# Performance work log

Measured on AMD Instinct MI355X. Metric: run time of the kernel, lower is better.

The kernel has to match this reference:

```python
import jax, jax.numpy as jnp
import numpy as np

N_CLASSES = 91  # classes 0..90; class 0 (background) is excluded from the mean


def setup_inputs() -> dict:
    key = jax.random.key(0)
    k1, k2 = jax.random.split(key)
    B, H, W = 64, 512, 512
    # label maps with integer class ids in [0, 91); `inputs` stored as float32
    # to mirror the original (compared elementwise against integer i)
    inputs = jax.random.randint(k1, (B, H, W), 0, N_CLASSES).astype(jnp.float32)
    targets = jax.random.randint(k2, (B, H, W), 0, N_CLASSES).astype(jnp.int32)
    return {"inputs": inputs, "targets": targets, "smooth": 1}


def reference(inputs, targets, smooth):
    # Single-pass histogram formulation of the original per-class loop:
    #   intersection_i = #{p : inputs[p]==i and targets[p]==i}
    #   total_i        = #{inputs==i} + #{targets==i}
    #   union_i        = total_i - intersection_i
    n = N_CLASSES
    inp = inputs.reshape(-1).astype(jnp.int32)
    tgt = targets.reshape(-1).astype(jnp.int32)
    cnt_in = jnp.bincount(inp, length=n).astype(jnp.float32)
    cnt_tg = jnp.bincount(tgt, length=n).astype(jnp.float32)
    # positions where prediction == target contribute to that class's intersection;
    # mismatches are routed to a dummy bin n and dropped
    inter = jnp.bincount(jnp.where(inp == tgt, inp, n), length=n + 1)[:n].astype(jnp.float32)
    union = cnt_in + cnt_tg - inter
    smooth_f = jnp.float32(smooth)
    iou = (inter[1:] + smooth_f) / (union[1:] + smooth_f)  # classes 1..n-1
    return jnp.sum(iou) / (n - 1)
```

## Files before the change

### kernel.cpp

```cpp
#include <hip/hip_runtime.h>

#define NCLS 91
#define NP (NCLS * NCLS)
#define NHIST (3 * NCLS)
#define NBLK 1024
#define BS 512

__device__ __forceinline__ void proc4(unsigned int* __restrict__ ph, float4 f, int4 t) {
    int a0 = (int)f.x, a1 = (int)f.y, a2 = (int)f.z, a3 = (int)f.w;
    atomicAdd(&ph[a0 * NCLS + t.x], 1u);
    atomicAdd(&ph[a1 * NCLS + t.y], 1u);
    atomicAdd(&ph[a2 * NCLS + t.z], 1u);
    atomicAdd(&ph[a3 * NCLS + t.w], 1u);
}

__global__ __launch_bounds__(BS, 8) void miou_hist(const float* __restrict__ inp,
                                                   const int* __restrict__ tgt,
                                                   unsigned int* __restrict__ ws,
                                                   int n4) {
    __shared__ unsigned int ph[NP];
    for (int i = threadIdx.x; i < NP; i += BS) ph[i] = 0u;
    __syncthreads();

    int tid = blockIdx.x * BS + threadIdx.x;
    int stride = gridDim.x * BS;
    const float4* in4 = (const float4*)inp;
    const int4* tg4 = (const int4*)tgt;

    int i = tid;
    for (; i + stride < n4; i += 2 * stride) {
        float4 f0 = in4[i];
        int4 t0 = tg4[i];
        float4 f1 = in4[i + stride];
        int4 t1 = tg4[i + stride];
        proc4(ph, f0, t0);
        proc4(ph, f1, t1);
    }
    if (i < n4) proc4(ph, in4[i], tg4[i]);
    __syncthreads();

    int t = threadIdx.x;
    if (t < NCLS) {
        unsigned int s = 0;
        const unsigned int* p = ph + t * NCLS;
        for (int k = 0; k < NCLS; ++k) s += p[k];
        if (s) atomicAdd(&ws[t], s);
    } else if (t >= 128 && t < 128 + NCLS) {
        int c = t - 128;
        unsigned int s = 0;
        for (int a = 0; a < NCLS; ++a) s += ph[a * NCLS + c];
        if (s) atomicAdd(&ws[NCLS + c], s);
    } else if (t >= 256 && t < 256 + NCLS) {
        int d = t - 256;
        unsigned int v = ph[d * (NCLS + 1)];
        if (v) atomicAdd(&ws[2 * NCLS + d], v);
    }
}

__global__ void miou_finalize(const unsigned int* __restrict__ ws,
                              const int* __restrict__ smooth_p,
                              float* __restrict__ out) {
    int lane = threadIdx.x;
    float s = (float)(*smooth_p);
    float acc = 0.f;
    for (int c = 1 + lane; c < NCLS; c += 64) {
        float ci = (float)ws[c];
        float ct = (float)ws[NCLS + c];
        float it = (float)ws[2 * NCLS + c];
        float un = ci + ct - it;
        acc += (it + s) / (un + s);
    }
    #pragma unroll
    for (int off = 32; off; off >>= 1) acc += __shfl_down(acc, off);
    if (lane == 0) out[0] = acc / (float)(NCLS - 1);
}

extern "C" void kernel_launch(void* const* d_in, const int* in_sizes, int n_in,
                              void* d_out, int out_size, void* d_ws, size_t ws_size,
                              hipStream_t stream) {
    const float* inp = (const float*)d_in[0];
    const int* tgt = (const int*)d_in[1];
    const int* smooth_p = (const int*)d_in[2];
    float* out = (float*)d_out;
    unsigned int* ws = (unsigned int*)d_ws;

    int n = in_sizes[0];
    int n4 = n >> 2;

    hipMemsetAsync(ws, 0, NHIST * sizeof(unsigned int), stream);
    miou_hist<<<NBLK, BS, 0, stream>>>(inp, tgt, ws, n4);
    miou_finalize<<<1, 64, 0, stream>>>(ws, smooth_p, out);
}
```

Measured before the change: 167.3 us.

## Halve block size, double-buffer batched loads, and restructure histogram reduction

The block size drops to 256 and each thread processes 16 strided float4/int4 pairs, loaded in two register buffers so one batch of global loads is in flight while the previous batch is scattered into the shared 91x91 histogram. Scheduling barriers group the global loads. Zeroing of shared memory is vectorised over a padded array, and the epilogue folds the diagonal extraction into the row-sum threads with 4-way unrolled partial sums. The tradeoff is more register pressure and fewer threads per block contending on the same LDS histogram. The fast path assumes 16*stride covers the data and falls back to a scalar loop otherwise.

```diff
diff --git a/kernel.cpp b/kernel.cpp
--- a/kernel.cpp
+++ b/kernel.cpp
@@ -2,9 +2,10 @@
 
 #define NCLS 91
 #define NP (NCLS * NCLS)
+#define NPPAD 8320
 #define NHIST (3 * NCLS)
 #define NBLK 1024
-#define BS 512
+#define BS 256
 
 __device__ __forceinline__ void proc4(unsigned int* __restrict__ ph, float4 f, int4 t) {
     int a0 = (int)f.x, a1 = (int)f.y, a2 = (int)f.z, a3 = (int)f.w;
@@ -14,46 +15,84 @@
     atomicAdd(&ph[a3 * NCLS + t.w], 1u);
 }
 
-__global__ __launch_bounds__(BS, 8) void miou_hist(const float* __restrict__ inp,
+__global__ __launch_bounds__(BS, 4) void miou_hist(const float* __restrict__ inp,
                                                    const int* __restrict__ tgt,
                                                    unsigned int* __restrict__ ws,
                                                    int n4) {
-    __shared__ unsigned int ph[NP];
-    for (int i = threadIdx.x; i < NP; i += BS) ph[i] = 0u;
+    __shared__ unsigned int ph[NPPAD];
+    uint4* z = (uint4*)ph;
+    #pragma unroll 2
+    for (int i = threadIdx.x; i < NPPAD / 4; i += BS) z[i] = make_uint4(0u, 0u, 0u, 0u);
     __syncthreads();
 
-    int tid = blockIdx.x * BS + threadIdx.x;
-    int stride = gridDim.x * BS;
     const float4* in4 = (const float4*)inp;
     const int4* tg4 = (const int4*)tgt;
+    const int i0 = blockIdx.x * BS + threadIdx.x;
+    const int stride = NBLK * BS;
 
-    int i = tid;
-    for (; i + stride < n4; i += 2 * stride) {
-        float4 f0 = in4[i];
-        int4 t0 = tg4[i];
-        float4 f1 = in4[i + stride];
-        int4 t1 = tg4[i + stride];
-        proc4(ph, f0, t0);
-        proc4(ph, f1, t1);
+    float4 fa0, fa1, fa2, fa3, fb0, fb1, fb2, fb3;
+    int4 ta0, ta1, ta2, ta3, tb0, tb1, tb2, tb3;
+
+#define LOADC(B, C)                                                         \
+    do {                                                                    \
+        int _b = i0 + (C) * 4 * stride;                                     \
+        f##B##0 = in4[_b];              t##B##0 = tg4[_b];                  \
+        f##B##1 = in4[_b + stride];     t##B##1 = tg4[_b + stride];         \
+        f##B##2 = in4[_b + 2 * stride]; t##B##2 = tg4[_b + 2 * stride];     \
+        f##B##3 = in4[_b + 3 * stride]; t##B##3 = tg4[_b + 3 * stride];     \
+        __builtin_amdgcn_sched_group_barrier(0x20, 8, 0);  \
+    } while (0)
+
+#define PROC(B)                                                             \
+    do {                                                                    \
+        proc4(ph, f##B##0, t##B##0);                                        \
+        proc4(ph, f##B##1, t##B##1);                                        \
+        proc4(ph, f##B##2, t##B##2);                                        \
+        proc4(ph, f##B##3, t##B##3);                                        \
+    } while (0)
+
+    int i = i0;
+    if (i0 + 15 * stride < n4) {
+        LOADC(a, 0);
+        LOADC(b, 1);
+        PROC(a);
+        LOADC(a, 2);
+        PROC(b);
+        LOADC(b, 3);
+        PROC(a);
+        PROC(b);
+        i = i0 + 16 * stride;
     }
-    if (i < n4) proc4(ph, in4[i], tg4[i]);
+    for (; i < n4; i += stride) proc4(ph, in4[i], tg4[i]);
+#undef LOADC
+#undef PROC
+
     __syncthreads();
 
     int t = threadIdx.x;
     if (t < NCLS) {
-        unsigned int s = 0;
         const unsigned int* p = ph + t * NCLS;
-        for (int k = 0; k < NCLS; ++k) s += p[k];
+        unsigned int s0 = 0, s1 = 0, s2 = 0, s3 = 0;
+        int k = 0;
+        for (; k + 3 < NCLS; k += 4) { s0 += p[k]; s1 += p[k+1]; s2 += p[k+2]; s3 += p[k+3]; }
+        for (; k < NCLS; ++k) s0 += p[k];
+        unsigned int s = s0 + s1 + s2 + s3;
         if (s) atomicAdd(&ws[t], s);
+        unsigned int d = p[t];
+        if (d) atomicAdd(&ws[2 * NCLS + t], d);
     } else if (t >= 128 && t < 128 + NCLS) {
         int c = t - 128;
-        unsigned int s = 0;
-        for (int a = 0; a < NCLS; ++a) s += ph[a * NCLS + c];
+        unsigned int s0 = 0, s1 = 0, s2 = 0, s3 = 0;
+        int a = 0;
+        for (; a + 3 < NCLS; a += 4) {
+            s0 += ph[a * NCLS + c];
+            s1 += ph[(a + 1) * NCLS + c];
+            s2 += ph[(a + 2) * NCLS + c];
+            s3 += ph[(a + 3) * NCLS + c];
+        }
+        for (; a < NCLS; ++a) s0 += ph[a * NCLS + c];
+        unsigned int s = s0 + s1 + s2 + s3;
         if (s) atomicAdd(&ws[NCLS + c], s);
-    } else if (t >= 256 && t < 256 + NCLS) {
-        int d = t - 256;
-        unsigned int v = ph[d * (NCLS + 1)];
-        if (v) atomicAdd(&ws[2 * NCLS + d], v);
     }
 }
 
```

Result: faster. 160.3 us (-4.2%).
